# Performance work log

Measured on AMD Instinct MI355X. Metric: run time of the kernel, lower is better.

## Reference

```python
import jax, jax.numpy as jnp
import numpy as np


def _degree_norms(src, dst, n_nodes):
    ones = jnp.ones(src.shape[0], dtype=jnp.float32)
    deg_out = jax.ops.segment_sum(ones, src, num_segments=n_nodes)
    deg_in = jax.ops.segment_sum(ones, dst, num_segments=n_nodes)
    # DGL GraphConv clamps degrees to min 1 before pow(-0.5)
    norm_src = jnp.power(jnp.maximum(deg_out, 1.0), -0.5)
    norm_dst = jnp.power(jnp.maximum(deg_in, 1.0), -0.5)
    return norm_src, norm_dst


def _graph_conv(h, src, dst, norm_src, norm_dst, W, b, activation):
    n_nodes = h.shape[0]
    # norm='both': scale source features, project, aggregate, scale dest
    x = h * norm_src[:, None]
    x = x @ W                                   # [N, out]
    m = x[src]                                  # gather  [E, out]
    agg = jax.ops.segment_sum(m, dst, num_segments=n_nodes)  # scatter-add [N, out]
    out = agg * norm_dst[:, None] + b
    if activation is not None:
        out = activation(out)
    return out


def setup_inputs() -> dict:
    key = jax.random.key(0)
    k = jax.random.split(key, 6)
    N, E, F, D = 100000, 1600000, 128, 128
    feature = jax.random.normal(k[0], (N, F), dtype=jnp.float32)
    src = jax.random.randint(k[1], (E,), 0, N, dtype=jnp.int32)
    dst = jax.random.randint(k[2], (E,), 0, N, dtype=jnp.int32)
    W1 = jax.random.normal(k[3], (F, D), dtype=jnp.float32) / np.sqrt(F)
    b1 = jnp.zeros((D,), dtype=jnp.float32)
    W2 = jax.random.normal(k[4], (D, D), dtype=jnp.float32) / np.sqrt(D)
    b2 = jnp.zeros((D,), dtype=jnp.float32)
    return {"feature": feature, "src": src, "dst": dst,
            "W1": W1, "b1": b1, "W2": W2, "b2": b2}


def reference(feature, src, dst, W1, b1, W2, b2):
    n_nodes = feature.shape[0]
    norm_src, norm_dst = _degree_norms(src, dst, n_nodes)
    # layer 0: relu; layer 1 (last): no activation
    h = _graph_conv(feature, src, dst, norm_src, norm_dst, W1, b1, jax.nn.relu)
    h = _graph_conv(h, src, dst, norm_src, norm_dst, W2, b2, None)
    return h
```

## Files before the change

kernel.cpp:

```cpp
#include <hip/hip_runtime.h>


#define RS_LOG 10
#define RS (1 << RS_LOG)

typedef short bf16x8 __attribute__((ext_vector_type(8)));
typedef float f32x4 __attribute__((ext_vector_type(4)));

__device__ __forceinline__ unsigned short rne_bf16(float v) {
  unsigned u = __float_as_uint(v);
  return (unsigned short)((u + 0x7FFF + ((u >> 16) & 1)) >> 16);
}

__global__ void build_graph(const int* __restrict__ src, const int* __restrict__ dst,
                            int* __restrict__ cursor, int* __restrict__ deg_out,
                            int* __restrict__ padded, int E, int CAP) {
  int e = blockIdx.x * blockDim.x + threadIdx.x;
  if (e < E) {
    int s = src[e];
    int d = dst[e];
    atomicAdd(&deg_out[s], 1);
    int pos = atomicAdd(&cursor[d], 1);
    if (pos < CAP) padded[(size_t)d * CAP + pos] = s;
  }
}

__global__ __launch_bounds__(256) void partition_edges(
    const int* __restrict__ src, const int* __restrict__ dst, int* __restrict__ g_cnt,
    int* __restrict__ part_dst, unsigned short* __restrict__ part_src, int E, int NR, int CAPR,
    int EPB) {
  __shared__ int cntD[256], cntS[256], baseD[256], baseS[256];
  int t = threadIdx.x;
  int e0 = blockIdx.x * EPB;
  int e1 = min(e0 + EPB, E);
  for (int i = t; i < NR; i += 256) {
    cntD[i] = 0;
    cntS[i] = 0;
  }
  __syncthreads();
  for (int e = e0 + t; e < e1; e += 256) {
    atomicAdd(&cntD[dst[e] >> RS_LOG], 1);
    atomicAdd(&cntS[src[e] >> RS_LOG], 1);
  }
  __syncthreads();
  for (int i = t; i < NR; i += 256) {
    baseD[i] = atomicAdd(&g_cnt[i * 16], cntD[i]);
    baseS[i] = atomicAdd(&g_cnt[(NR + i) * 16], cntS[i]);
    cntD[i] = 0;
    cntS[i] = 0;
  }
  __syncthreads();
  for (int e = e0 + t; e < e1; e += 256) {
    int s = src[e];
    int d = dst[e];
    int rd = d >> RS_LOG;
    int rs = s >> RS_LOG;
    int pd = baseD[rd] + atomicAdd(&cntD[rd], 1);
    if (pd < CAPR) part_dst[(size_t)rd * CAPR + pd] = ((d & (RS - 1)) << 17) | s;
    int ps = baseS[rs] + atomicAdd(&cntS[rs], 1);
    if (ps < CAPR) part_src[(size_t)rs * CAPR + ps] = (unsigned short)(s & (RS - 1));
  }
}

__global__ __launch_bounds__(512) void build_structures(
    const int* __restrict__ g_cnt, const int* __restrict__ part_dst,
    const unsigned short* __restrict__ part_src, int* __restrict__ padded,
    int* __restrict__ deg_in, int* __restrict__ deg_out, int N, int NR, int CAPR, int CAP) {
  __shared__ int cur[RS];
  int t = threadIdx.x;
  int b = blockIdx.x;
  for (int i = t; i < RS; i += 512) cur[i] = 0;
  __syncthreads();
  if (b < NR) {
    int cnt = min(g_cnt[b * 16], CAPR);
    const int* p = part_dst + (size_t)b * CAPR;
    for (int i = t; i < cnt; i += 512) {
      int v = p[i];
      int dlow = v >> 17;
      int s = v & 0x1FFFF;
      int pos = atomicAdd(&cur[dlow], 1);
      if (pos < CAP) padded[((size_t)((b << RS_LOG) + dlow)) * CAP + pos] = s;
    }
    __syncthreads();
    int nbase = b << RS_LOG;
    for (int i = t; i < RS; i += 512) {
      int node = nbase + i;
      if (node < N) deg_in[node] = cur[i];
    }
  } else {
    int r = b - NR;
    int cnt = min(g_cnt[(NR + r) * 16], CAPR);
    const unsigned short* p = part_src + (size_t)r * CAPR;
    for (int i = t; i < cnt; i += 512) atomicAdd(&cur[p[i]], 1);
    __syncthreads();
    int nbase = r << RS_LOG;
    for (int i = t; i < RS; i += 512) {
      int node = nbase + i;
      if (node < N) deg_out[node] = cur[i];
    }
  }
}

__global__ void compute_norms(const int* __restrict__ deg_out, const int* __restrict__ deg_in,
                              float* __restrict__ norm_src, float* __restrict__ norm_dst, int N) {
  int i = blockIdx.x * blockDim.x + threadIdx.x;
  if (i < N) {
    norm_src[i] = rsqrtf((float)max(deg_out[i], 1));
    norm_dst[i] = rsqrtf((float)max(deg_in[i], 1));
  }
}

__global__ __launch_bounds__(256) void prep_w(const float* __restrict__ W,
                                              unsigned short* __restrict__ Wt_hi,
                                              unsigned short* __restrict__ Wt_lo) {
  int idx = blockIdx.x * 256 + threadIdx.x;
  int k = idx >> 7;
  int c = idx & 127;
  float w = W[idx];
  unsigned short h = rne_bf16(w);
  float hf = __uint_as_float((unsigned)h << 16);
  unsigned short l = rne_bf16(w - hf);
  Wt_hi[c * 128 + k] = h;
  Wt_lo[c * 128 + k] = l;
}

__global__ __launch_bounds__(256) void gemm_mfma(const float* __restrict__ X,
                                                 const unsigned short* __restrict__ Wt_hi,
                                                 const unsigned short* __restrict__ Wt_lo,
                                                 const float* __restrict__ norm,
                                                 unsigned short* __restrict__ Ybf, int N) {
  int t = threadIdx.x;
  int lane = t & 63;
  int wv = t >> 6;
  int r0 = blockIdx.x * 128;
  int c = lane & 15;
  int kgrp = lane >> 4;

  int rowA0 = r0 + wv * 32 + c;
  int rowA1 = rowA0 + 16;
  bool ok0 = rowA0 < N;
  bool ok1 = rowA1 < N;
  float nn0 = ok0 ? norm[rowA0] : 0.f;
  float nn1 = ok1 ? norm[rowA1] : 0.f;
  const float* xr0 = X + (size_t)rowA0 * 128;
  const float* xr1 = X + (size_t)rowA1 * 128;
  const unsigned short* pbh = Wt_hi + (size_t)c * 128;
  const unsigned short* pbl = Wt_lo + (size_t)c * 128;

  f32x4 acc[2][8];
#pragma unroll
  for (int mr = 0; mr < 2; mr++)
#pragma unroll
    for (int nr = 0; nr < 8; nr++) acc[mr][nr] = (f32x4){0.f, 0.f, 0.f, 0.f};

#pragma unroll
  for (int s = 0; s < 4; s++) {
    int kb = s * 32 + kgrp * 8;
    bf16x8 ah[2], al[2];
    {
      float4 z = make_float4(0.f, 0.f, 0.f, 0.f);
      float4 x0a = ok0 ? *(const float4*)(xr0 + kb) : z;
      float4 x0b = ok0 ? *(const float4*)(xr0 + kb + 4) : z;
      float4 x1a = ok1 ? *(const float4*)(xr1 + kb) : z;
      float4 x1b = ok1 ? *(const float4*)(xr1 + kb + 4) : z;
      float v0[8] = {x0a.x, x0a.y, x0a.z, x0a.w, x0b.x, x0b.y, x0b.z, x0b.w};
      float v1[8] = {x1a.x, x1a.y, x1a.z, x1a.w, x1b.x, x1b.y, x1b.z, x1b.w};
#pragma unroll
      for (int j = 0; j < 8; j++) {
        float a = v0[j] * nn0;
        unsigned short h = rne_bf16(a);
        ah[0][j] = (short)h;
        al[0][j] = (short)rne_bf16(a - __uint_as_float((unsigned)h << 16));
        float b = v1[j] * nn1;
        unsigned short h2 = rne_bf16(b);
        ah[1][j] = (short)h2;
        al[1][j] = (short)rne_bf16(b - __uint_as_float((unsigned)h2 << 16));
      }
    }
#pragma unroll
    for (int nr = 0; nr < 8; nr++) {
      bf16x8 bh = *(const bf16x8*)(pbh + nr * 2048 + kb);
      bf16x8 bl = *(const bf16x8*)(pbl + nr * 2048 + kb);
#pragma unroll
      for (int mr = 0; mr < 2; mr++) {
        acc[mr][nr] = __builtin_amdgcn_mfma_f32_16x16x32_bf16(ah[mr], bh, acc[mr][nr], 0, 0, 0);
        acc[mr][nr] = __builtin_amdgcn_mfma_f32_16x16x32_bf16(al[mr], bh, acc[mr][nr], 0, 0, 0);
        acc[mr][nr] = __builtin_amdgcn_mfma_f32_16x16x32_bf16(ah[mr], bl, acc[mr][nr], 0, 0, 0);
      }
    }
  }

#pragma unroll
  for (int mr = 0; mr < 2; mr++) {
    int rb = r0 + wv * 32 + mr * 16 + kgrp * 4;
#pragma unroll
    for (int q = 0; q < 4; q++) {
      int row = rb + q;
      if (row < N) {
        unsigned short* yo = Ybf + (size_t)row * 128 + c;
#pragma unroll
        for (int nr = 0; nr < 8; nr++) yo[nr * 16] = rne_bf16(acc[mr][nr][q]);
      }
    }
  }
}

__global__ __launch_bounds__(256) void spmm_bf(const unsigned* __restrict__ Ybf,
                                               const int* __restrict__ padded,
                                               const int* __restrict__ deg_in,
                                               const float* __restrict__ norm_dst,
                                               const float* __restrict__ bias,
                                               float* __restrict__ out, int N, int CAP,
                                               int do_relu) {
  int t = threadIdx.x;
  int lane = t & 63;
  int wv = t >> 6;
  int v = blockIdx.x * 4 + wv;
  if (v >= N) return;
  int cnt = min(deg_in[v], CAP);
  int sidx = (lane < cnt) ? padded[(size_t)v * CAP + lane] : 0;
  float ax = 0.f, ay = 0.f;
  int i = 0;
  for (; i + 4 <= cnt; i += 4) {
    int s0 = __builtin_amdgcn_readlane(sidx, i);
    int s1 = __builtin_amdgcn_readlane(sidx, i + 1);
    int s2 = __builtin_amdgcn_readlane(sidx, i + 2);
    int s3 = __builtin_amdgcn_readlane(sidx, i + 3);
    unsigned w0 = Ybf[(size_t)s0 * 64 + lane];
    unsigned w1 = Ybf[(size_t)s1 * 64 + lane];
    unsigned w2 = Ybf[(size_t)s2 * 64 + lane];
    unsigned w3 = Ybf[(size_t)s3 * 64 + lane];
    ax += __uint_as_float(w0 << 16) + __uint_as_float(w1 << 16) +
          __uint_as_float(w2 << 16) + __uint_as_float(w3 << 16);
    ay += __uint_as_float(w0 & 0xFFFF0000u) + __uint_as_float(w1 & 0xFFFF0000u) +
          __uint_as_float(w2 & 0xFFFF0000u) + __uint_as_float(w3 & 0xFFFF0000u);
  }
  for (; i < cnt; i++) {
    int s = __builtin_amdgcn_readlane(sidx, i);
    unsigned w = Ybf[(size_t)s * 64 + lane];
    ax += __uint_as_float(w << 16);
    ay += __uint_as_float(w & 0xFFFF0000u);
  }
  float nd = norm_dst[v];
  float2 b = ((const float2*)bias)[lane];
  float2 r;
  r.x = ax * nd + b.x;
  r.y = ay * nd + b.y;
  if (do_relu) {
    r.x = fmaxf(r.x, 0.f);
    r.y = fmaxf(r.y, 0.f);
  }
  ((float2*)out)[(size_t)v * 64 + lane] = r;
}

extern "C" void kernel_launch(void* const* d_in, const int* in_sizes, int n_in,
                              void* d_out, int out_size, void* d_ws, size_t ws_size,
                              hipStream_t stream) {
  const float* feature = (const float*)d_in[0];
  const int* src = (const int*)d_in[1];
  const int* dst = (const int*)d_in[2];
  const float* W1 = (const float*)d_in[3];
  const float* b1 = (const float*)d_in[4];
  const float* W2 = (const float*)d_in[5];
  const float* b2 = (const float*)d_in[6];
  float* out = (float*)d_out;

  const int F = 128;
  int N = in_sizes[0] / F;
  int E = in_sizes[1];
  (void)n_in;
  (void)out_size;

  char* ws = (char*)d_ws;
  size_t off = 0;
  auto alloc = [&](size_t bytes) -> char* {
    char* p = ws + off;
    off = (off + bytes + 255) & ~(size_t)255;
    return p;
  };
  float* h_buf = (float*)alloc((size_t)N * F * 4);
  int* degs = (int*)alloc((size_t)2 * N * 4);
  int* deg_in_ = degs;
  int* deg_out_ = degs + N;
  float* norm_src = (float*)alloc((size_t)N * 4);
  float* norm_dst = (float*)alloc((size_t)N * 4);
  unsigned short* wt1_hi = (unsigned short*)alloc(128 * 128 * 2);
  unsigned short* wt1_lo = (unsigned short*)alloc(128 * 128 * 2);
  unsigned short* wt2_hi = (unsigned short*)alloc(128 * 128 * 2);
  unsigned short* wt2_lo = (unsigned short*)alloc(128 * 128 * 2);

  int NR = (N + RS - 1) >> RS_LOG;
  int CAPR = (E + NR - 1) / NR + 4096;
  CAPR = (CAPR + 31) & ~31;
  size_t part_bytes =
      (size_t)NR * CAPR * 4 + (size_t)NR * CAPR * 2 + (size_t)2 * NR * 16 * 4 + 1024;
  size_t avail = (ws_size > off) ? ws_size - off : 0;

  int CAP;
  bool partition_ok = (N <= 131072) && (NR <= 256);
  bool use_part;
  if (partition_ok && avail >= (size_t)N * 64 * 4 + part_bytes) {
    CAP = 64;
    use_part = true;
  } else if (partition_ok && avail >= (size_t)N * 48 * 4 + part_bytes) {
    CAP = 48;
    use_part = true;
  } else if (avail >= (size_t)N * 64 * 4 + (size_t)N * 4 + 256) {
    CAP = 64;
    use_part = false;
  } else if (avail >= (size_t)N * 48 * 4 + (size_t)N * 4 + 256) {
    CAP = 48;
    use_part = false;
  } else {
    CAP = 32;
    use_part = false;
  }
  int* padded = (int*)alloc((size_t)N * CAP * 4);

  prep_w<<<64, 256, 0, stream>>>(W1, wt1_hi, wt1_lo);
  prep_w<<<64, 256, 0, stream>>>(W2, wt2_hi, wt2_lo);

  if (use_part) {
    int* part_dst = (int*)alloc((size_t)NR * CAPR * 4);
    unsigned short* part_src = (unsigned short*)alloc((size_t)NR * CAPR * 2);
    int* g_cnt = (int*)alloc((size_t)2 * NR * 16 * 4);
    const int EPB = 4096;
    int NB = (E + EPB - 1) / EPB;
    hipMemsetAsync(g_cnt, 0, (size_t)2 * NR * 16 * 4, stream);
    partition_edges<<<NB, 256, 0, stream>>>(src, dst, g_cnt, part_dst, part_src, E, NR, CAPR,
                                            EPB);
    build_structures<<<2 * NR, 512, 0, stream>>>(g_cnt, part_dst, part_src, padded, deg_in_,
                                                 deg_out_, N, NR, CAPR, CAP);
  } else {
    int* cursor = (int*)alloc((size_t)N * 4);
    hipMemsetAsync(degs, 0, (size_t)2 * N * 4, stream);
    build_graph<<<(E + 255) / 256, 256, 0, stream>>>(src, dst, deg_in_, deg_out_, padded, E, CAP);
    (void)cursor;
  }
  compute_norms<<<(N + 255) / 256, 256, 0, stream>>>(deg_out_, deg_in_, norm_src, norm_dst, N);

  unsigned short* ybf1 = (unsigned short*)d_out;
  unsigned short* ybf2;
  float* final_target;
  bool need_copy;
  size_t ybf_bytes = (size_t)N * 128 * 2;
  if (ws_size > off && ws_size - off >= ybf_bytes + 256) {
    ybf2 = (unsigned short*)alloc(ybf_bytes);
    final_target = out;
    need_copy = false;
  } else {
    ybf2 = (unsigned short*)d_out;
    final_target = h_buf;
    need_copy = true;
  }

  int gblocks = (N + 127) / 128;
  gemm_mfma<<<gblocks, 256, 0, stream>>>(feature, wt1_hi, wt1_lo, norm_src, ybf1, N);
  spmm_bf<<<(N + 3) / 4, 256, 0, stream>>>((const unsigned*)ybf1, padded, deg_in_, norm_dst, b1,
                                           h_buf, N, CAP, 1);
  gemm_mfma<<<gblocks, 256, 0, stream>>>(h_buf, wt2_hi, wt2_lo, norm_src, ybf2, N);
  spmm_bf<<<(N + 3) / 4, 256, 0, stream>>>((const unsigned*)ybf2, padded, deg_in_, norm_dst, b2,
                                           final_target, N, CAP, 0);
  if (need_copy) {
    hipMemcpyAsync(out, h_buf, (size_t)N * F * 4, hipMemcpyDeviceToDevice, stream);
  }
}
```

Baseline: 414.1 us.

## Stage GEMM input rows into swizzled LDS via direct global-to-LDS loads

The projection GEMM now stages its 64-row fp32 input tile into shared memory with global_load_lds 16-byte transfers, using an XOR swizzle to avoid bank conflicts. Each wave then handles 16 rows instead of 32, so the block tile halves and the grid doubles, with a launch_bounds occupancy hint. The goal is to replace strided per-lane global reads with coalesced bulk loads and raise occupancy. The cost is one full vmcnt wait plus barrier before any compute, with no overlap, and the per-block reads of the W fragments are now amortised over fewer rows.

```diff
diff --git a/kernel.cpp b/kernel.cpp
--- a/kernel.cpp
+++ b/kernel.cpp
@@ -10,6 +10,11 @@
 __device__ __forceinline__ unsigned short rne_bf16(float v) {
   unsigned u = __float_as_uint(v);
   return (unsigned short)((u + 0x7FFF + ((u >> 16) & 1)) >> 16);
+}
+
+__device__ __forceinline__ void load_lds16(const void* g, void* l) {
+  __builtin_amdgcn_global_load_lds((const __attribute__((address_space(1))) unsigned*)g,
+                                   (__attribute__((address_space(3))) unsigned*)l, 16, 0, 0);
 }
 
 __global__ void build_graph(const int* __restrict__ src, const int* __restrict__ dst,
@@ -124,83 +129,79 @@
   Wt_lo[c * 128 + k] = l;
 }
 
-__global__ __launch_bounds__(256) void gemm_mfma(const float* __restrict__ X,
-                                                 const unsigned short* __restrict__ Wt_hi,
-                                                 const unsigned short* __restrict__ Wt_lo,
-                                                 const float* __restrict__ norm,
-                                                 unsigned short* __restrict__ Ybf, int N) {
+__global__ __launch_bounds__(256, 4) void gemm_mfma_lds(const float* __restrict__ X,
+                                                        const unsigned short* __restrict__ Wt_hi,
+                                                        const unsigned short* __restrict__ Wt_lo,
+                                                        const float* __restrict__ norm,
+                                                        unsigned short* __restrict__ Ybf, int N) {
+  __shared__ unsigned char XlB[32768] __attribute__((aligned(128)));
   int t = threadIdx.x;
   int lane = t & 63;
   int wv = t >> 6;
-  int r0 = blockIdx.x * 128;
+  int l = lane;
+  int tile_r0 = blockIdx.x * 64;
+  long valid_bytes = ((long)N - tile_r0) * 512;
+
+  const char* xbase = (const char*)X + (size_t)tile_r0 * 512;
+#pragma unroll
+  for (int j = 0; j < 8; j++) {
+    int d = j * 4096 + wv * 1024 + l * 16;
+    int off = d ^ (((d >> 9) & 7) << 4);
+    if (off >= valid_bytes) off = 0;
+    load_lds16(xbase + off, XlB + j * 4096 + wv * 1024);
+  }
+  asm volatile("s_waitcnt vmcnt(0)" ::: "memory");
+  __syncthreads();
+
   int c = lane & 15;
   int kgrp = lane >> 4;
-
-  int rowA0 = r0 + wv * 32 + c;
-  int rowA1 = rowA0 + 16;
-  bool ok0 = rowA0 < N;
-  bool ok1 = rowA1 < N;
-  float nn0 = ok0 ? norm[rowA0] : 0.f;
-  float nn1 = ok1 ? norm[rowA1] : 0.f;
-  const float* xr0 = X + (size_t)rowA0 * 128;
-  const float* xr1 = X + (size_t)rowA1 * 128;
+  int rowA = tile_r0 + wv * 16 + c;
+  bool okA = rowA < N;
+  float nn = okA ? norm[rowA] : 0.f;
   const unsigned short* pbh = Wt_hi + (size_t)c * 128;
   const unsigned short* pbl = Wt_lo + (size_t)c * 128;
 
-  f32x4 acc[2][8];
-#pragma unroll
-  for (int mr = 0; mr < 2; mr++)
-#pragma unroll
-    for (int nr = 0; nr < 8; nr++) acc[mr][nr] = (f32x4){0.f, 0.f, 0.f, 0.f};
+  f32x4 acc[8];
+#pragma unroll
+  for (int nr = 0; nr < 8; nr++) acc[nr] = (f32x4){0.f, 0.f, 0.f, 0.f};
 
 #pragma unroll
   for (int s = 0; s < 4; s++) {
     int kb = s * 32 + kgrp * 8;
-    bf16x8 ah[2], al[2];
+    int rloc = wv * 16 + c;
+    int byteA = rloc * 512 + kb * 4;
+    int a0 = byteA ^ ((rloc & 7) << 4);
+    float4 xa = *(const float4*)(XlB + a0);
+    float4 xb = *(const float4*)(XlB + (a0 ^ 16));
+    bf16x8 ah, al;
     {
-      float4 z = make_float4(0.f, 0.f, 0.f, 0.f);
-      float4 x0a = ok0 ? *(const float4*)(xr0 + kb) : z;
-      float4 x0b = ok0 ? *(const float4*)(xr0 + kb + 4) : z;
-      float4 x1a = ok1 ? *(const float4*)(xr1 + kb) : z;
-      float4 x1b = ok1 ? *(const float4*)(xr1 + kb + 4) : z;
-      float v0[8] = {x0a.x, x0a.y, x0a.z, x0a.w, x0b.x, x0b.y, x0b.z, x0b.w};
-      float v1[8] = {x1a.x, x1a.y, x1a.z, x1a.w, x1b.x, x1b.y, x1b.z, x1b.w};
+      float v[8] = {xa.x, xa.y, xa.z, xa.w, xb.x, xb.y, xb.z, xb.w};
 #pragma unroll
       for (int j = 0; j < 8; j++) {
-        float a = v0[j] * nn0;
+        float a = v[j] * nn;
         unsigned short h = rne_bf16(a);
-        ah[0][j] = (short)h;
-        al[0][j] = (short)rne_bf16(a - __uint_as_float((unsigned)h << 16));
-        float b = v1[j] * nn1;
-        unsigned short h2 = rne_bf16(b);
-        ah[1][j] = (short)h2;
-        al[1][j] = (short)rne_bf16(b - __uint_as_float((unsigned)h2 << 16));
+        ah[j] = (short)h;
+        al[j] = (short)rne_bf16(a - __uint_as_float((unsigned)h << 16));
       }
     }
 #pragma unroll
     for (int nr = 0; nr < 8; nr++) {
       bf16x8 bh = *(const bf16x8*)(pbh + nr * 2048 + kb);
       bf16x8 bl = *(const bf16x8*)(pbl + nr * 2048 + kb);
-#pragma unroll
-      for (int mr = 0; mr < 2; mr++) {
-        acc[mr][nr] = __builtin_amdgcn_mfma_f32_16x16x32_bf16(ah[mr], bh, acc[mr][nr], 0, 0, 0);
-        acc[mr][nr] = __builtin_amdgcn_mfma_f32_16x16x32_bf16(al[mr], bh, acc[mr][nr], 0, 0, 0);
-        acc[mr][nr] = __builtin_amdgcn_mfma_f32_16x16x32_bf16(ah[mr], bl, acc[mr][nr], 0, 0, 0);
-      }
-    }
-  }
-
-#pragma unroll
-  for (int mr = 0; mr < 2; mr++) {
-    int rb = r0 + wv * 32 + mr * 16 + kgrp * 4;
-#pragma unroll
-    for (int q = 0; q < 4; q++) {
-      int row = rb + q;
-      if (row < N) {
-        unsigned short* yo = Ybf + (size_t)row * 128 + c;
-#pragma unroll
-        for (int nr = 0; nr < 8; nr++) yo[nr * 16] = rne_bf16(acc[mr][nr][q]);
-      }
+      acc[nr] = __builtin_amdgcn_mfma_f32_16x16x32_bf16(ah, bh, acc[nr], 0, 0, 0);
+      acc[nr] = __builtin_amdgcn_mfma_f32_16x16x32_bf16(al, bh, acc[nr], 0, 0, 0);
+      acc[nr] = __builtin_amdgcn_mfma_f32_16x16x32_bf16(ah, bl, acc[nr], 0, 0, 0);
+    }
+  }
+
+  int rb = tile_r0 + wv * 16 + kgrp * 4;
+#pragma unroll
+  for (int q = 0; q < 4; q++) {
+    int row = rb + q;
+    if (row < N) {
+      unsigned short* yo = Ybf + (size_t)row * 128 + c;
+#pragma unroll
+      for (int nr = 0; nr < 8; nr++) yo[nr * 16] = rne_bf16(acc[nr][q]);
     }
   }
 }
@@ -354,11 +355,11 @@
     need_copy = true;
   }
 
-  int gblocks = (N + 127) / 128;
-  gemm_mfma<<<gblocks, 256, 0, stream>>>(feature, wt1_hi, wt1_lo, norm_src, ybf1, N);
+  int gblocks = (N + 63) / 64;
+  gemm_mfma_lds<<<gblocks, 256, 0, stream>>>(feature, wt1_hi, wt1_lo, norm_src, ybf1, N);
   spmm_bf<<<(N + 3) / 4, 256, 0, stream>>>((const unsigned*)ybf1, padded, deg_in_, norm_dst, b1,
                                            h_buf, N, CAP, 1);
-  gemm_mfma<<<gblocks, 256, 0, stream>>>(h_buf, wt2_hi, wt2_lo, norm_src, ybf2, N);
+  gemm_mfma_lds<<<gblocks, 256, 0, stream>>>(h_buf, wt2_hi, wt2_lo, norm_src, ybf2, N);
   spmm_bf<<<(N + 3) / 4, 256, 0, stream>>>((const unsigned*)ybf2, padded, deg_in_, norm_dst, b2,
                                            final_target, N, CAP, 0);
   if (need_copy) {
```

New measurement: 410.9 us. Within noise of the previous version (-0.8%).
